# Kernel tuning notes

Measured on AMD Instinct MI355X. Metric: run time of the kernel, lower is better.

Reference implementation:

```python
import jax, jax.numpy as jnp
import numpy as np
from jax import lax

L, B, D = 2048, 16, 1024

def setup_inputs() -> dict:
    key = jax.random.key(0)
    k1, k2, k3 = jax.random.split(key, 3)
    prev_layer = jax.random.normal(k1, (L, B, D), dtype=jnp.float32)
    hidden = jax.random.normal(k2, (B, D), dtype=jnp.float32)
    W = jax.random.normal(k3, (3 * D, D), dtype=jnp.float32) * (1.0 / np.sqrt(D))
    b = jnp.zeros((3 * D,), dtype=jnp.float32)
    return {"prev_layer": prev_layer, "hidden": hidden, "W": W, "b": b}

def reference(prev_layer, hidden, W, b):
    # prev_layer: [L, B, D], hidden: [B, D], W: [3D, D], b: [3D]
    d = hidden.shape[-1]
    # nn.Linear: y = x @ W.T + b  (dropout p=0 -> identity)
    preact = jnp.einsum('lbi,oi->lbo', prev_layer, W) + b  # [L, B, 3D]
    x_t = preact[..., :d]                                   # candidate
    gates = jax.nn.sigmoid(preact[..., d:])                 # [L, B, 2D]
    z = gates[..., :d]
    h_gate = gates[..., d:]

    def step(h, zx):
        zt, xt = zx
        s = (1.0 - zt) * h + zt * xt
        return s, s

    hidden_final, ss = lax.scan(step, hidden, (z, x_t))     # ss: [L, B, D]
    out = (1.0 - h_gate) * ss + h_gate * prev_layer         # highway (input_size==output_size)
    return out, hidden_final
```

## Files before the change

### kernel.cpp

```cpp
#include <hip/hip_runtime.h>
#include <cstdint>

#define L_DIM 2048
#define B_DIM 16
#define D_DIM 1024
#define M_DIM (L_DIM*B_DIM)
#define N_DIM (3*D_DIM)
#define K_DIM D_DIM
#define NCH   (B_DIM*D_DIM)
#define SEG   64
#define SEGLEN (L_DIM/SEG)
#define CG    (NCH/8)

typedef __bf16 bf16x8 __attribute__((ext_vector_type(8)));
typedef float f32x4 __attribute__((ext_vector_type(4)));

__device__ inline float bf2f(ushort u){ return __uint_as_float(((unsigned)u)<<16); }
__device__ inline ushort f2bf(float f){
  unsigned u = __float_as_uint(f);
  u += 0x7fffu + ((u>>16)&1u);
  return (ushort)(u>>16);
}

__global__ __launch_bounds__(256) void cvt8(const float* __restrict__ in,
                                            ushort* __restrict__ out, int n8){
  int t = blockIdx.x*256 + threadIdx.x;
  if (t >= n8) return;
  const float4* p = (const float4*)(in + (size_t)t*8);
  float4 a = p[0], b = p[1];
  ushort r[8] = {f2bf(a.x),f2bf(a.y),f2bf(a.z),f2bf(a.w),
                 f2bf(b.x),f2bf(b.y),f2bf(b.z),f2bf(b.w)};
  *(uint4*)(out + (size_t)t*8) = *(const uint4*)r;
}

__global__ __launch_bounds__(256) void gemm_sru(
    const ushort* __restrict__ A,
    const ushort* __restrict__ Bt,
    const float* __restrict__ bias,
    ushort* __restrict__ xbuf, ushort* __restrict__ zbuf, ushort* __restrict__ hbuf)
{
  __shared__ ushort As[128*32];
  __shared__ ushort Bs[128*32];
  const int tid  = threadIdx.x;
  const int lane = tid & 63, w = tid >> 6;
  const int wm = w >> 1, wn = w & 1;
  const int bnb = blockIdx.x % (N_DIM/128);
  const int bmb = blockIdx.x / (N_DIM/128);
  const int bm = bmb*128, bn = bnb*128;

  f32x4 acc[4][4];
  #pragma unroll
  for (int i=0;i<4;i++)
    #pragma unroll
    for (int j=0;j<4;j++) acc[i][j] = (f32x4){0.f,0.f,0.f,0.f};

  const int lrow = lane & 15, lk = (lane>>4)*8;

  for (int k0 = 0; k0 < K_DIM; k0 += 32) {
    #pragma unroll
    for (int q=0;q<2;q++){
      int c = (w*2+q)*64 + lane;
      int row = c >> 2, k8 = (c&3)*8;
      __builtin_amdgcn_global_load_lds(
        (const __attribute__((address_space(1))) void*)(A + (size_t)(bm+row)*K_DIM + k0 + k8),
        (__attribute__((address_space(3))) void*)(As + c*8), 16, 0, 0);
      __builtin_amdgcn_global_load_lds(
        (const __attribute__((address_space(1))) void*)(Bt + (size_t)(bn+row)*K_DIM + k0 + k8),
        (__attribute__((address_space(3))) void*)(Bs + c*8), 16, 0, 0);
    }
    __syncthreads();

    bf16x8 af[4], bf[4];
    #pragma unroll
    for (int i=0;i<4;i++) af[i] = *(const bf16x8*)(As + (wm*64 + i*16 + lrow)*32 + lk);
    #pragma unroll
    for (int j=0;j<4;j++) bf[j] = *(const bf16x8*)(Bs + (wn*64 + j*16 + lrow)*32 + lk);
    #pragma unroll
    for (int i=0;i<4;i++)
      #pragma unroll
      for (int j=0;j<4;j++)
        acc[i][j] = __builtin_amdgcn_mfma_f32_16x16x32_bf16(af[i], bf[j], acc[i][j], 0,0,0);
    __syncthreads();
  }

  const int region = bn >> 10;
  ushort* dst = region==0 ? xbuf : (region==1 ? zbuf : hbuf);
  #pragma unroll
  for (int j=0;j<4;j++){
    int o = bn + wn*64 + j*16 + lrow;
    float bv = bias[o];
    int colr = o & (D_DIM-1);
    #pragma unroll
    for (int i=0;i<4;i++){
      #pragma unroll
      for (int r=0;r<4;r++){
        int m = bm + wm*64 + i*16 + (lane>>4)*4 + r;
        float v = acc[i][j][r] + bv;
        if (region) v = 1.f/(1.f + __expf(-v));
        dst[(size_t)m*D_DIM + colr] = f2bf(v);
      }
    }
  }
}

__global__ __launch_bounds__(256) void scan_pass1(
    const ushort* __restrict__ z, const ushort* __restrict__ x,
    float* __restrict__ Aout, float* __restrict__ Bout)
{
  int t = blockIdx.x*256 + threadIdx.x;
  int cg = t & (CG-1), g = t >> 11;
  int c0 = cg*8;
  size_t base = (size_t)g*SEGLEN*NCH + c0;
  float A[8], Bc[8];
  #pragma unroll
  for (int j=0;j<8;j++){ A[j]=1.f; Bc[j]=0.f; }
  #pragma unroll 4
  for (int i=0;i<SEGLEN;i++){
    uint4 zv = *(const uint4*)(z + base + (size_t)i*NCH);
    uint4 xv = *(const uint4*)(x + base + (size_t)i*NCH);
    const ushort* zp = (const ushort*)&zv;
    const ushort* xp = (const ushort*)&xv;
    #pragma unroll
    for (int j=0;j<8;j++){
      float zf = bf2f(zp[j]);
      float a  = 1.f - zf;
      float b  = zf * bf2f(xp[j]);
      Bc[j] = a*Bc[j] + b;
      A[j]  = a*A[j];
    }
  }
  float* Ao = Aout + (size_t)g*NCH + c0;
  float* Bo = Bout + (size_t)g*NCH + c0;
  *(float4*)Ao     = make_float4(A[0],A[1],A[2],A[3]);
  *(float4*)(Ao+4) = make_float4(A[4],A[5],A[6],A[7]);
  *(float4*)Bo     = make_float4(Bc[0],Bc[1],Bc[2],Bc[3]);
  *(float4*)(Bo+4) = make_float4(Bc[4],Bc[5],Bc[6],Bc[7]);
}

__global__ __launch_bounds__(256) void scan_pass2(
    const float* __restrict__ A, const float* __restrict__ B,
    const float* __restrict__ h0, float* __restrict__ seg, float* __restrict__ hfin)
{
  int c = blockIdx.x*256 + threadIdx.x;
  float s = h0[c];
  #pragma unroll 8
  for (int g=0; g<SEG; g++){
    seg[(size_t)g*NCH + c] = s;
    s = A[(size_t)g*NCH + c]*s + B[(size_t)g*NCH + c];
  }
  hfin[c] = s;
}

__global__ __launch_bounds__(256) void scan_pass3(
    const ushort* __restrict__ z, const ushort* __restrict__ x, const ushort* __restrict__ hg,
    const float* __restrict__ prev, const float* __restrict__ seg,
    float* __restrict__ out)
{
  int t = blockIdx.x*256 + threadIdx.x;
  int cg = t & (CG-1), g = t >> 11;
  int c0 = cg*8;
  float s[8];
  *(float4*)s     = *(const float4*)(seg + (size_t)g*NCH + c0);
  *(float4*)(s+4) = *(const float4*)(seg + (size_t)g*NCH + c0 + 4);
  size_t base = (size_t)g*SEGLEN*NCH + c0;
  #pragma unroll 2
  for (int i=0;i<SEGLEN;i++){
    size_t idx = base + (size_t)i*NCH;
    uint4 zv = *(const uint4*)(z+idx);
    uint4 xv = *(const uint4*)(x+idx);
    uint4 hv = *(const uint4*)(hg+idx);
    float4 p0 = *(const float4*)(prev+idx);
    float4 p1 = *(const float4*)(prev+idx+4);
    const ushort* zp=(const ushort*)&zv;
    const ushort* xp=(const ushort*)&xv;
    const ushort* hp=(const ushort*)&hv;
    float pv[8] = {p0.x,p0.y,p0.z,p0.w,p1.x,p1.y,p1.z,p1.w};
    float o[8];
    #pragma unroll
    for (int j=0;j<8;j++){
      float zf = bf2f(zp[j]);
      s[j] += zf*(bf2f(xp[j]) - s[j]);
      float hf = bf2f(hp[j]);
      o[j] = s[j] + hf*(pv[j] - s[j]);
    }
    *(float4*)(out+idx)   = make_float4(o[0],o[1],o[2],o[3]);
    *(float4*)(out+idx+4) = make_float4(o[4],o[5],o[6],o[7]);
  }
}

extern "C" void kernel_launch(void* const* d_in, const int* in_sizes, int n_in,
                              void* d_out, int out_size, void* d_ws, size_t ws_size,
                              hipStream_t stream) {
  const float* prev = (const float*)d_in[0];
  const float* h0   = (const float*)d_in[1];
  const float* W    = (const float*)d_in[2];
  const float* bias = (const float*)d_in[3];
  float* out  = (float*)d_out;
  float* hfin = out + (size_t)M_DIM*D_DIM;

  char* ws = (char*)d_ws;
  ushort* Ab = (ushort*)ws;
  ushort* Wb = (ushort*)(ws + (size_t)M_DIM*K_DIM*2);
  ushort* xb = (ushort*)(ws + (size_t)M_DIM*K_DIM*2 + (size_t)N_DIM*K_DIM*2);
  ushort* zb = xb + (size_t)M_DIM*D_DIM;
  ushort* hb = zb + (size_t)M_DIM*D_DIM;
  float* Abuf = (float*)ws;
  float* Bbuf = Abuf + (size_t)SEG*NCH;
  float* segb = Bbuf + (size_t)SEG*NCH;

  cvt8<<<(M_DIM*K_DIM/8 + 255)/256, 256, 0, stream>>>(prev, Ab, M_DIM*K_DIM/8);
  cvt8<<<(N_DIM*K_DIM/8 + 255)/256, 256, 0, stream>>>(W,    Wb, N_DIM*K_DIM/8);
  gemm_sru<<<(M_DIM/128)*(N_DIM/128), 256, 0, stream>>>(Ab, Wb, bias, xb, zb, hb);
  scan_pass1<<<(CG*SEG)/256, 256, 0, stream>>>(zb, xb, Abuf, Bbuf);
  scan_pass2<<<NCH/256, 256, 0, stream>>>(Abuf, Bbuf, h0, segb, hfin);
  scan_pass3<<<(CG*SEG)/256, 256, 0, stream>>>(zb, xb, hb, prev, segb, out);
}
```

Measured before the change: 434.0 us.

## Rewrite GEMM with 256x256 tiles, double-buffered LDS, swizzling and staged epilogue

The bf16 GEMM moves from 128x128 tiles with 256 threads and single-buffered BK=32 to 256x256 tiles with 1024 threads, BK=64 and a double-buffered 128KB LDS pipeline that prefetches the next K tile while MFMAs run. It adds XOR swizzling of LDS rows to avoid bank conflicts, a block-id remap for L2 locality, and s_setprio around the MFMA bursts. The epilogue stages bf16 results through LDS so global stores become coalesced 16-byte writes. The 128KB of LDS and 1024-thread blocks limit occupancy to one block per CU, and the launch_bounds occupancy hint may not be achievable.

```diff
diff --git a/kernel.cpp b/kernel.cpp
--- a/kernel.cpp
+++ b/kernel.cpp
@@ -12,6 +12,10 @@
 #define SEGLEN (L_DIM/SEG)
 #define CG    (NCH/8)
 
+#define BK 64
+#define NKT (K_DIM/BK)
+#define BUF 65536
+
 typedef __bf16 bf16x8 __attribute__((ext_vector_type(8)));
 typedef float f32x4 __attribute__((ext_vector_type(4)));
 
@@ -33,20 +37,37 @@
   *(uint4*)(out + (size_t)t*8) = *(const uint4*)r;
 }
 
-__global__ __launch_bounds__(256) void gemm_sru(
-    const ushort* __restrict__ A,
-    const ushort* __restrict__ Bt,
+#define GLOAD(gp, lp) __builtin_amdgcn_global_load_lds( \
+    (const __attribute__((address_space(1))) void*)(gp), \
+    (__attribute__((address_space(3))) void*)(lp), 16, 0, 0)
+
+__global__ __launch_bounds__(1024, 4) void gemm_sru(
+    const ushort* __restrict__ gA,
+    const ushort* __restrict__ gB,
     const float* __restrict__ bias,
     ushort* __restrict__ xbuf, ushort* __restrict__ zbuf, ushort* __restrict__ hbuf)
 {
-  __shared__ ushort As[128*32];
-  __shared__ ushort Bs[128*32];
+  __shared__ ulong2 lds_[2*BUF/16];
+  char* ldsb = (char*)lds_;
+
   const int tid  = threadIdx.x;
   const int lane = tid & 63, w = tid >> 6;
-  const int wm = w >> 1, wn = w & 1;
-  const int bnb = blockIdx.x % (N_DIM/128);
-  const int bmb = blockIdx.x / (N_DIM/128);
-  const int bm = bmb*128, bn = bnb*128;
+  const int wr = (w>>2)*64;
+  const int wc = (w&3)*64;
+
+  const int bid = blockIdx.x;
+  const int swz = (bid & 7)*192 + (bid >> 3);
+  const int bm = (swz / (N_DIM/256))*256, bn = (swz % (N_DIM/256))*256;
+
+  const int l15 = lane & 15, l4 = lane >> 4;
+  const int s0 = ((l4)     ^ (l15&7)) * 16;
+  const int s1 = ((4 + l4) ^ (l15&7)) * 16;
+  const char* pA = ldsb + (wr + l15)*128;
+  const char* pB = ldsb + 32768 + (wc + l15)*128;
+
+  const int gsl = (tid & 7) ^ ((tid >> 3) & 7);
+  const ushort* gAp = gA + (size_t)(bm + (tid>>3))*K_DIM + gsl*8;
+  const ushort* gBp = gB + (size_t)(bn + (tid>>3))*K_DIM + gsl*8;
 
   f32x4 acc[4][4];
   #pragma unroll
@@ -54,53 +75,110 @@
     #pragma unroll
     for (int j=0;j<4;j++) acc[i][j] = (f32x4){0.f,0.f,0.f,0.f};
 
-  const int lrow = lane & 15, lk = (lane>>4)*8;
-
-  for (int k0 = 0; k0 < K_DIM; k0 += 32) {
-    #pragma unroll
-    for (int q=0;q<2;q++){
-      int c = (w*2+q)*64 + lane;
-      int row = c >> 2, k8 = (c&3)*8;
-      __builtin_amdgcn_global_load_lds(
-        (const __attribute__((address_space(1))) void*)(A + (size_t)(bm+row)*K_DIM + k0 + k8),
-        (__attribute__((address_space(3))) void*)(As + c*8), 16, 0, 0);
-      __builtin_amdgcn_global_load_lds(
-        (const __attribute__((address_space(1))) void*)(Bt + (size_t)(bn+row)*K_DIM + k0 + k8),
-        (__attribute__((address_space(3))) void*)(Bs + c*8), 16, 0, 0);
-    }
-    __syncthreads();
-
-    bf16x8 af[4], bf[4];
-    #pragma unroll
-    for (int i=0;i<4;i++) af[i] = *(const bf16x8*)(As + (wm*64 + i*16 + lrow)*32 + lk);
-    #pragma unroll
-    for (int j=0;j<4;j++) bf[j] = *(const bf16x8*)(Bs + (wn*64 + j*16 + lrow)*32 + lk);
-    #pragma unroll
-    for (int i=0;i<4;i++)
-      #pragma unroll
-      for (int j=0;j<4;j++)
-        acc[i][j] = __builtin_amdgcn_mfma_f32_16x16x32_bf16(af[i], bf[j], acc[i][j], 0,0,0);
+#define STAGE(tt) do{ \
+    char* d = ldsb + ((tt)&1)*BUF; \
+    GLOAD(gAp + (size_t)(tt)*BK,                  d + tid*16); \
+    GLOAD(gAp + (size_t)128*K_DIM + (size_t)(tt)*BK, d + 16384 + tid*16); \
+    GLOAD(gBp + (size_t)(tt)*BK,                  d + 32768 + tid*16); \
+    GLOAD(gBp + (size_t)128*K_DIM + (size_t)(tt)*BK, d + 49152 + tid*16); \
+  }while(0)
+
+  STAGE(0);
+  __syncthreads();
+
+  for (int t = 0; t < NKT; ++t) {
+    const int bo = (t&1)*BUF;
+    if (t < NKT-1) STAGE(t+1);
+
+    bf16x8 a0 = *(const bf16x8*)(pA + bo + 0*2048 + s0);
+    bf16x8 a1 = *(const bf16x8*)(pA + bo + 1*2048 + s0);
+    bf16x8 a2 = *(const bf16x8*)(pA + bo + 2*2048 + s0);
+    bf16x8 a3 = *(const bf16x8*)(pA + bo + 3*2048 + s0);
+    bf16x8 b0 = *(const bf16x8*)(pB + bo + 0*2048 + s0);
+    bf16x8 b1 = *(const bf16x8*)(pB + bo + 1*2048 + s0);
+    bf16x8 b2 = *(const bf16x8*)(pB + bo + 2*2048 + s0);
+    bf16x8 b3 = *(const bf16x8*)(pB + bo + 3*2048 + s0);
+    __builtin_amdgcn_s_setprio(1);
+    acc[0][0] = __builtin_amdgcn_mfma_f32_16x16x32_bf16(a0, b0, acc[0][0], 0,0,0);
+    acc[0][1] = __builtin_amdgcn_mfma_f32_16x16x32_bf16(a0, b1, acc[0][1], 0,0,0);
+    acc[0][2] = __builtin_amdgcn_mfma_f32_16x16x32_bf16(a0, b2, acc[0][2], 0,0,0);
+    acc[0][3] = __builtin_amdgcn_mfma_f32_16x16x32_bf16(a0, b3, acc[0][3], 0,0,0);
+    acc[1][0] = __builtin_amdgcn_mfma_f32_16x16x32_bf16(a1, b0, acc[1][0], 0,0,0);
+    acc[1][1] = __builtin_amdgcn_mfma_f32_16x16x32_bf16(a1, b1, acc[1][1], 0,0,0);
+    acc[1][2] = __builtin_amdgcn_mfma_f32_16x16x32_bf16(a1, b2, acc[1][2], 0,0,0);
+    acc[1][3] = __builtin_amdgcn_mfma_f32_16x16x32_bf16(a1, b3, acc[1][3], 0,0,0);
+    acc[2][0] = __builtin_amdgcn_mfma_f32_16x16x32_bf16(a2, b0, acc[2][0], 0,0,0);
+    acc[2][1] = __builtin_amdgcn_mfma_f32_16x16x32_bf16(a2, b1, acc[2][1], 0,0,0);
+    acc[2][2] = __builtin_amdgcn_mfma_f32_16x16x32_bf16(a2, b2, acc[2][2], 0,0,0);
+    acc[2][3] = __builtin_amdgcn_mfma_f32_16x16x32_bf16(a2, b3, acc[2][3], 0,0,0);
+    acc[3][0] = __builtin_amdgcn_mfma_f32_16x16x32_bf16(a3, b0, acc[3][0], 0,0,0);
+    acc[3][1] = __builtin_amdgcn_mfma_f32_16x16x32_bf16(a3, b1, acc[3][1], 0,0,0);
+    acc[3][2] = __builtin_amdgcn_mfma_f32_16x16x32_bf16(a3, b2, acc[3][2], 0,0,0);
+    acc[3][3] = __builtin_amdgcn_mfma_f32_16x16x32_bf16(a3, b3, acc[3][3], 0,0,0);
+    __builtin_amdgcn_s_setprio(0);
+
+    a0 = *(const bf16x8*)(pA + bo + 0*2048 + s1);
+    a1 = *(const bf16x8*)(pA + bo + 1*2048 + s1);
+    a2 = *(const bf16x8*)(pA + bo + 2*2048 + s1);
+    a3 = *(const bf16x8*)(pA + bo + 3*2048 + s1);
+    b0 = *(const bf16x8*)(pB + bo + 0*2048 + s1);
+    b1 = *(const bf16x8*)(pB + bo + 1*2048 + s1);
+    b2 = *(const bf16x8*)(pB + bo + 2*2048 + s1);
+    b3 = *(const bf16x8*)(pB + bo + 3*2048 + s1);
+    __builtin_amdgcn_s_setprio(1);
+    acc[0][0] = __builtin_amdgcn_mfma_f32_16x16x32_bf16(a0, b0, acc[0][0], 0,0,0);
+    acc[0][1] = __builtin_amdgcn_mfma_f32_16x16x32_bf16(a0, b1, acc[0][1], 0,0,0);
+    acc[0][2] = __builtin_amdgcn_mfma_f32_16x16x32_bf16(a0, b2, acc[0][2], 0,0,0);
+    acc[0][3] = __builtin_amdgcn_mfma_f32_16x16x32_bf16(a0, b3, acc[0][3], 0,0,0);
+    acc[1][0] = __builtin_amdgcn_mfma_f32_16x16x32_bf16(a1, b0, acc[1][0], 0,0,0);
+    acc[1][1] = __builtin_amdgcn_mfma_f32_16x16x32_bf16(a1, b1, acc[1][1], 0,0,0);
+    acc[1][2] = __builtin_amdgcn_mfma_f32_16x16x32_bf16(a1, b2, acc[1][2], 0,0,0);
+    acc[1][3] = __builtin_amdgcn_mfma_f32_16x16x32_bf16(a1, b3, acc[1][3], 0,0,0);
+    acc[2][0] = __builtin_amdgcn_mfma_f32_16x16x32_bf16(a2, b0, acc[2][0], 0,0,0);
+    acc[2][1] = __builtin_amdgcn_mfma_f32_16x16x32_bf16(a2, b1, acc[2][1], 0,0,0);
+    acc[2][2] = __builtin_amdgcn_mfma_f32_16x16x32_bf16(a2, b2, acc[2][2], 0,0,0);
+    acc[2][3] = __builtin_amdgcn_mfma_f32_16x16x32_bf16(a2, b3, acc[2][3], 0,0,0);
+    acc[3][0] = __builtin_amdgcn_mfma_f32_16x16x32_bf16(a3, b0, acc[3][0], 0,0,0);
+    acc[3][1] = __builtin_amdgcn_mfma_f32_16x16x32_bf16(a3, b1, acc[3][1], 0,0,0);
+    acc[3][2] = __builtin_amdgcn_mfma_f32_16x16x32_bf16(a3, b2, acc[3][2], 0,0,0);
+    acc[3][3] = __builtin_amdgcn_mfma_f32_16x16x32_bf16(a3, b3, acc[3][3], 0,0,0);
+    __builtin_amdgcn_s_setprio(0);
+
     __syncthreads();
   }
 
   const int region = bn >> 10;
   ushort* dst = region==0 ? xbuf : (region==1 ? zbuf : hbuf);
-  #pragma unroll
-  for (int j=0;j<4;j++){
-    int o = bn + wn*64 + j*16 + lrow;
-    float bv = bias[o];
-    int colr = o & (D_DIM-1);
-    #pragma unroll
-    for (int i=0;i<4;i++){
+  ushort* lds16 = (ushort*)ldsb;
+  float bv[4];
+  #pragma unroll
+  for (int g=0; g<4; ++g) bv[g] = bias[bn + wc + g*16 + l15];
+
+  #pragma unroll
+  for (int f=0; f<4; ++f)
+    #pragma unroll
+    for (int g=0; g<4; ++g)
       #pragma unroll
-      for (int r=0;r<4;r++){
-        int m = bm + wm*64 + i*16 + (lane>>4)*4 + r;
-        float v = acc[i][j][r] + bv;
+      for (int r=0; r<4; ++r){
+        int row = wr + f*16 + l4*4 + r;
+        int col = wc + g*16 + l15;
+        float v = acc[f][g][r] + bv[g];
         if (region) v = 1.f/(1.f + __expf(-v));
-        dst[(size_t)m*D_DIM + colr] = f2bf(v);
+        int slot = col >> 3;
+        lds16[row*256 + (((slot ^ (row&31))&31)<<3) + (col&7)] = f2bf(v);
       }
-    }
-  }
+  __syncthreads();
+  const int cb = bn & (D_DIM-1);
+  #pragma unroll
+  for (int i=0;i<8;i++){
+    int off = i*16384 + tid*16;
+    int row = off >> 9;
+    int slot = (off >> 4) & 31;
+    int dcol = (off & 511) >> 1;
+    const char* src = ldsb + row*512 + (((slot ^ (row&31))&31)<<4);
+    *(uint4*)(dst + (size_t)(bm+row)*D_DIM + cb + dcol) = *(const uint4*)src;
+  }
+#undef STAGE
 }
 
 __global__ __launch_bounds__(256) void scan_pass1(
@@ -124,8 +202,8 @@
     for (int j=0;j<8;j++){
       float zf = bf2f(zp[j]);
       float a  = 1.f - zf;
-      float b  = zf * bf2f(xp[j]);
-      Bc[j] = a*Bc[j] + b;
+      float bb = zf * bf2f(xp[j]);
+      Bc[j] = a*Bc[j] + bb;
       A[j]  = a*A[j];
     }
   }
@@ -210,7 +288,7 @@
 
   cvt8<<<(M_DIM*K_DIM/8 + 255)/256, 256, 0, stream>>>(prev, Ab, M_DIM*K_DIM/8);
   cvt8<<<(N_DIM*K_DIM/8 + 255)/256, 256, 0, stream>>>(W,    Wb, N_DIM*K_DIM/8);
-  gemm_sru<<<(M_DIM/128)*(N_DIM/128), 256, 0, stream>>>(Ab, Wb, bias, xb, zb, hb);
+  gemm_sru<<<(M_DIM/256)*(N_DIM/256), 1024, 0, stream>>>(Ab, Wb, bias, xb, zb, hb);
   scan_pass1<<<(CG*SEG)/256, 256, 0, stream>>>(zb, xb, Abuf, Bbuf);
   scan_pass2<<<NCH/256, 256, 0, stream>>>(Abuf, Bbuf, h0, segb, hfin);
   scan_pass3<<<(CG*SEG)/256, 256, 0, stream>>>(zb, xb, hb, prev, segb, out);
```

Result: faster. 391.3 us (-9.8%).
